# Optimization experiments

Hardware: AMD Instinct MI355X
Metric: run time of the kernel (lower is better)

## Reference

```python
import jax, jax.numpy as jnp
import numpy as np
import math

D_EMBED, D_K, N_HEADS = 1024, 1024, 16
D_H = D_EMBED // N_HEADS          # 64
ROT_DIM = D_H // 2                # 32, RotaryEmbedding(dim=d_h//2)
B, LQ, LK = 2, 2048, 2048


def _rope_freqs(seq_len):
    # lucidrains rotary-embedding-torch: inv_freq over half of `dim`, interleave-repeated
    inv_freq = 1.0 / (10000.0 ** (jnp.arange(0, ROT_DIM, 2, dtype=jnp.float32) / ROT_DIM))
    t = jnp.arange(seq_len, dtype=jnp.float32)
    f = t[:, None] * inv_freq[None, :]          # [S, ROT_DIM/2]
    return jnp.repeat(f, 2, axis=-1)            # [S, ROT_DIM] interleaved


def _apply_rotary(x, freqs):
    # x: [B,H,S,D_H]; rotate first ROT_DIM features, pass the rest through
    x_rot, x_pass = x[..., :ROT_DIM], x[..., ROT_DIM:]
    cos, sin = jnp.cos(freqs), jnp.sin(freqs)   # [S, ROT_DIM]
    x1, x2 = x_rot[..., 0::2], x_rot[..., 1::2]
    rotated = jnp.stack((-x2, x1), axis=-1).reshape(x_rot.shape)
    return jnp.concatenate([x_rot * cos + rotated * sin, x_pass], axis=-1)


def setup_inputs() -> dict:
    key = jax.random.key(0)
    ks = jax.random.split(key, 12)
    s = 0.02
    return {
        "embed": jax.random.normal(ks[0], (B, LQ, D_EMBED), jnp.float32),
        "key": jax.random.normal(ks[1], (B, LK, D_K), jnp.float32),
        "attn_mask": jnp.ones((B, LQ, LK), dtype=bool),
        "WQ": jax.random.normal(ks[2], (D_EMBED, D_EMBED), jnp.float32) * s,
        "bQ": jnp.zeros((D_EMBED,), jnp.float32),
        "WK": jax.random.normal(ks[3], (D_K, D_EMBED), jnp.float32) * s,
        "bK": jnp.zeros((D_EMBED,), jnp.float32),
        "WV": jax.random.normal(ks[4], (D_K, D_EMBED), jnp.float32) * s,
        "bV": jnp.zeros((D_EMBED,), jnp.float32),
        "WO": jax.random.normal(ks[5], (D_EMBED, D_EMBED), jnp.float32) * s,
        "bO": jnp.zeros((D_EMBED,), jnp.float32),
    }


def reference(embed, key, attn_mask, WQ, bQ, WK, bK, WV, bV, WO, bO):
    bsz, len_q, _ = embed.shape
    len_k = key.shape[1]
    scale = 1.0 / math.sqrt(D_EMBED)  # note: module scales by 1/sqrt(d_embed)

    Q = embed @ WQ + bQ
    K = key @ WK + bK
    V = key @ WV + bV

    # [B, H, S, D_H]
    Qh = Q.reshape(bsz, len_q, N_HEADS, D_H).transpose(0, 2, 1, 3)
    Kh = K.reshape(bsz, len_k, N_HEADS, D_H).transpose(0, 2, 1, 3)
    Vh = V.reshape(bsz, len_k, N_HEADS, D_H).transpose(0, 2, 1, 3)

    Qh = _apply_rotary(Qh, _rope_freqs(len_q))
    Kh = _apply_rotary(Kh, _rope_freqs(len_k))

    attn = jnp.einsum('bhqd,bhkd->bhqk', Qh, Kh)
    attn = jnp.where(attn_mask[:, None, :, :], attn, -jnp.inf)
    attn = jax.nn.softmax(attn * scale, axis=-1)

    out = jnp.einsum('bhqk,bhkd->bhqd', attn, Vh)
    out = out.transpose(0, 2, 1, 3).reshape(bsz, len_q, D_EMBED)
    return out @ WO + bO
```

## Files before the change

kernel.cpp:

```cpp
#include <hip/hip_runtime.h>
#include <hip/hip_bf16.h>
#include <cstdint>
#include <cstddef>

typedef __bf16 bf16_t;
typedef bf16_t bf16x8 __attribute__((ext_vector_type(8)));
typedef bf16_t bf16x4 __attribute__((ext_vector_type(4)));
typedef bf16_t bf16x2 __attribute__((ext_vector_type(2)));
typedef float f32x4 __attribute__((ext_vector_type(4)));
typedef float f32x16 __attribute__((ext_vector_type(16)));
typedef unsigned int u32x4 __attribute__((ext_vector_type(4)));

namespace {
constexpr int Bv = 2, Lv = 2048, Ev = 1024, NHv = 16;
constexpr int Mv = Bv * Lv;
constexpr float SCALE_L2E = 0.03125f * 1.4426950408889634f;
}

__device__ __forceinline__ void gload_lds16(const void* g, void* l) {
  __builtin_amdgcn_global_load_lds(
      (const __attribute__((address_space(1))) unsigned int*)g,
      (__attribute__((address_space(3))) unsigned int*)l,
      16, 0, 0);
}

__global__ __launch_bounds__(256) void k_cvt2(const float* __restrict__ x0,
                                              const float* __restrict__ x1,
                                              bf16_t* __restrict__ y0,
                                              bf16_t* __restrict__ y1, int n4) {
  const float* x = blockIdx.z ? x1 : x0;
  bf16_t* y = blockIdx.z ? y1 : y0;
  int i = blockIdx.x * 256 + threadIdx.x;
  if (i < n4) {
    float4 v = reinterpret_cast<const float4*>(x)[i];
    bf16x4 o = {(bf16_t)v.x, (bf16_t)v.y, (bf16_t)v.z, (bf16_t)v.w};
    *reinterpret_cast<bf16x4*>(&y[(size_t)i * 4]) = o;
  }
}

__global__ __launch_bounds__(256) void k_twt(const float* w0, const float* w1,
                                             const float* w2, const float* w3,
                                             bf16_t* t0, bf16_t* t1,
                                             bf16_t* t2, bf16_t* t3) {
  const float* W;
  bf16_t* T;
  switch (blockIdx.z) {
    case 0: W = w0; T = t0; break;
    case 1: W = w1; T = t1; break;
    case 2: W = w2; T = t2; break;
    default: W = w3; T = t3; break;
  }
  __shared__ float tile[32][33];
  const int tx = threadIdx.x, ty = threadIdx.y;
  const int n0 = blockIdx.x * 32, k0 = blockIdx.y * 32;
#pragma unroll
  for (int i = 0; i < 4; i++) {
    int r = ty + i * 8;
    tile[r][tx] = W[(size_t)(k0 + r) * Ev + n0 + tx];
  }
  __syncthreads();
#pragma unroll
  for (int i = 0; i < 4; i++) {
    int r = ty + i * 8;
    T[(size_t)(n0 + r) * Ev + k0 + tx] = (bf16_t)tile[tx][r];
  }
}

__global__ __launch_bounds__(256) void k_trig(float2* __restrict__ tab) {
  int t = blockIdx.x * 256 + threadIdx.x;
  int i = t & 15, l = t >> 4;
  float inv = exp2f(-13.287712379549449f * (float)i * (1.0f / 16.0f));
  float s, c;
  sincosf((float)l * inv, &s, &c);
  tab[t] = make_float2(c, s);
}

__global__ __launch_bounds__(256) void k_gemm_qkv(
    const bf16_t* __restrict__ Ae, const bf16_t* __restrict__ Ak,
    const bf16_t* __restrict__ WtQ, const bf16_t* __restrict__ WtK,
    const bf16_t* __restrict__ WtV, const float* __restrict__ bQ,
    const float* __restrict__ bK, const float* __restrict__ bV,
    const float2* __restrict__ tab, bf16_t* __restrict__ Qbf,
    bf16_t* __restrict__ Kbf, bf16_t* __restrict__ Vtr) {
  constexpr int K = Ev;
  const int z = blockIdx.z;
  const bf16_t* A = (z == 0) ? Ae : Ak;
  const bf16_t* Bt = (z == 0) ? WtQ : (z == 1) ? WtK : WtV;
  const float* bias = (z == 0) ? bQ : (z == 1) ? bK : bV;

  __shared__ __align__(16) bf16_t As[128 * 32];
  __shared__ __align__(16) bf16_t Bs[128 * 32];
  const int tid = threadIdx.x;
  const int wid = tid >> 6, lane = tid & 63;
  const int bm = blockIdx.y * 128, bn = blockIdx.x * 128;
  const int wr = wid >> 1, wc = wid & 1;
  f32x4 acc[4][4] = {};
  const int srow = wid * 32 + (lane >> 2);
  const int scol = (lane & 3) * 8;
  const size_t ga0 = (size_t)(bm + srow) * K + scol;
  const size_t ga1 = (size_t)(bm + srow + 16) * K + scol;
  const size_t gb0 = (size_t)(bn + srow) * K + scol;
  const size_t gb1 = (size_t)(bn + srow + 16) * K + scol;
  bf16_t* asw = &As[wid * 1024];
  bf16_t* bsw = &Bs[wid * 1024];
  for (int k0 = 0; k0 < K; k0 += 32) {
    gload_lds16(A + ga0 + k0, asw);
    gload_lds16(A + ga1 + k0, asw + 512);
    gload_lds16(Bt + gb0 + k0, bsw);
    gload_lds16(Bt + gb1 + k0, bsw + 512);
    __syncthreads();
    bf16x8 af[4], bfr[4];
#pragma unroll
    for (int m = 0; m < 4; m++)
      af[m] = *(const bf16x8*)&As[(wr * 64 + m * 16 + (lane & 15)) * 32 + (lane >> 4) * 8];
#pragma unroll
    for (int n = 0; n < 4; n++)
      bfr[n] = *(const bf16x8*)&Bs[(wc * 64 + n * 16 + (lane & 15)) * 32 + (lane >> 4) * 8];
#pragma unroll
    for (int m = 0; m < 4; m++)
#pragma unroll
      for (int n = 0; n < 4; n++)
        acc[m][n] = __builtin_amdgcn_mfma_f32_16x16x32_bf16(af[m], bfr[n], acc[m][n], 0, 0, 0);
    __syncthreads();
  }

  const int l15 = lane & 15, g = lane >> 4;
  if (z == 2) {
#pragma unroll
    for (int n = 0; n < 4; n++) {
      const int col = bn + wc * 64 + n * 16 + l15;
      const int hh = (col >> 6) & 15;
      const int d = col & 63;
      const float bv = bias[col];
#pragma unroll
      for (int m = 0; m < 4; m++) {
        const int row0 = bm + wr * 64 + m * 16 + (g << 2);
        const int b = row0 >> 11, l0 = row0 & 2047;
        const int pq = (l0 >> 2) & 3;
        const int pq2 = ((pq & 1) << 1) | (pq >> 1);
        const int l0p = (l0 & ~12) | (pq2 << 2);
        bf16x4 ov;
#pragma unroll
        for (int r = 0; r < 4; r++) ov[r] = (bf16_t)(acc[m][n][r] + bv);
        *(bf16x4*)&Vtr[((size_t)((b * NHv + hh) * 64 + d)) * Lv + l0p] = ov;
      }
    }
    return;
  }

  bf16_t* Y = (z == 0) ? Qbf : Kbf;
  const float scale = (z == 0) ? SCALE_L2E : 1.0f;
  const float ssign = (l15 & 1) ? 1.0f : -1.0f;
#pragma unroll
  for (int n = 0; n < 4; n++) {
    const int col = bn + wc * 64 + n * 16 + l15;
    const int h = (col >> 6) & 15;
    const int d = col & 63;
    const float bv = bias[col];
    const bool dorope = (d < 32);
    const int ti = d >> 1;
#pragma unroll
    for (int m = 0; m < 4; m++) {
      const int row0 = bm + wr * 64 + m * 16 + (g << 2);
#pragma unroll
      for (int r = 0; r < 4; r++) {
        const int row = row0 + r;
        const int l = row & 2047, b = row >> 11;
        float v = acc[m][n][r] + bv;
        float p = __shfl_xor(v, 1);
        float o = v;
        if (dorope) {
          float2 cs = tab[(l << 4) + ti];
          o = v * cs.x + p * cs.y * ssign;
        }
        Y[(((size_t)(b * NHv + h)) * Lv + l) * 64 + d] = (bf16_t)(o * scale);
      }
    }
  }
}

__global__ __launch_bounds__(256) void k_gemm_bt(const bf16_t* __restrict__ A,
                                                 const bf16_t* __restrict__ Bt,
                                                 const float* __restrict__ bias,
                                                 float* __restrict__ C,
                                                 int N, int K) {
  __shared__ __align__(16) bf16_t As[128 * 32];
  __shared__ __align__(16) bf16_t Bs[128 * 32];
  const int tid = threadIdx.x;
  const int wid = tid >> 6, lane = tid & 63;
  const int bm = blockIdx.y * 128, bn = blockIdx.x * 128;
  const int wr = wid >> 1, wc = wid & 1;
  f32x4 acc[4][4] = {};
  const int srow = wid * 32 + (lane >> 2);
  const int scol = (lane & 3) * 8;
  const size_t ga0 = (size_t)(bm + srow) * K + scol;
  const size_t ga1 = (size_t)(bm + srow + 16) * K + scol;
  const size_t gb0 = (size_t)(bn + srow) * K + scol;
  const size_t gb1 = (size_t)(bn + srow + 16) * K + scol;
  bf16_t* asw = &As[wid * 1024];
  bf16_t* bsw = &Bs[wid * 1024];
  for (int k0 = 0; k0 < K; k0 += 32) {
    gload_lds16(A + ga0 + k0, asw);
    gload_lds16(A + ga1 + k0, asw + 512);
    gload_lds16(Bt + gb0 + k0, bsw);
    gload_lds16(Bt + gb1 + k0, bsw + 512);
    __syncthreads();
    bf16x8 af[4], bfr[4];
#pragma unroll
    for (int m = 0; m < 4; m++)
      af[m] = *(const bf16x8*)&As[(wr * 64 + m * 16 + (lane & 15)) * 32 + (lane >> 4) * 8];
#pragma unroll
    for (int n = 0; n < 4; n++)
      bfr[n] = *(const bf16x8*)&Bs[(wc * 64 + n * 16 + (lane & 15)) * 32 + (lane >> 4) * 8];
#pragma unroll
    for (int m = 0; m < 4; m++)
#pragma unroll
      for (int n = 0; n < 4; n++)
        acc[m][n] = __builtin_amdgcn_mfma_f32_16x16x32_bf16(af[m], bfr[n], acc[m][n], 0, 0, 0);
    __syncthreads();
  }
#pragma unroll
  for (int n = 0; n < 4; n++) {
    const int col = bn + wc * 64 + n * 16 + (lane & 15);
    const float bv = bias[col];
#pragma unroll
    for (int m = 0; m < 4; m++) {
      const int row0 = bm + wr * 64 + m * 16 + ((lane >> 4) << 2);
#pragma unroll
      for (int r = 0; r < 4; r++)
        C[(size_t)(row0 + r) * N + col] = acc[m][n][r] + bv;
    }
  }
}

__global__ void k_flag_init(int* f) { f[0] = 1; f[1] = 1; }

__global__ __launch_bounds__(256) void k_mask_and(const unsigned int* __restrict__ m,
                                                  int* __restrict__ f, int nwords) {
  int i = blockIdx.x * 256 + threadIdx.x;
  const int u8words = nwords >> 2;
  bool badA = false, badB = false;
  for (; i < nwords; i += gridDim.x * 256) {
    unsigned int v = m[i];
    badA |= (i < u8words) & (v != 0x01010101u);
    badB |= (v != 1u);
  }
  if (__any(badA) && (threadIdx.x & 63) == 0) f[0] = 0;
  if (__any(badB) && (threadIdx.x & 63) == 0) f[1] = 0;
}

__device__ __forceinline__ void flash_stage(const bf16_t* __restrict__ Kg,
                                            const bf16_t* __restrict__ Vg,
                                            bf16_t* ksb, bf16_t* vsb,
                                            int tid, int kt) {
#pragma unroll
  for (int i = 0; i < 2; i++) {
    int slot = i * 256 + tid;
    int r = slot >> 3, c = slot & 7;
    int sb = ((c * 16) ^ ((r & 7) << 4)) >> 1;
    bf16_t* dk = ksb + (size_t)(i * 256 + (tid & 192)) * 8;
    gload_lds16(Kg + (size_t)(kt * 64 + r) * 64 + sb, dk);
    bf16_t* dv = vsb + (size_t)(i * 256 + (tid & 192)) * 8;
    gload_lds16(Vg + (size_t)r * Lv + kt * 64 + sb, dv);
  }
}

__global__ __launch_bounds__(256) void k_flash32(const bf16_t* __restrict__ Qh,
                                                 const bf16_t* __restrict__ Kh,
                                                 const bf16_t* __restrict__ Vtr,
                                                 const int* __restrict__ mask,
                                                 const int* __restrict__ allflag,
                                                 bf16_t* __restrict__ Oh) {
  __shared__ __align__(16) bf16_t Ks[2][64 * 64];
  __shared__ __align__(16) bf16_t Vs[2][64 * 64];
  __shared__ float sw[4][32];
  const int tid = threadIdx.x, wid = tid >> 6, lane = tid & 63;
  const int l31 = lane & 31, hf = lane >> 5;
  const int bh = blockIdx.x, qt = blockIdx.y;
  const int b = bh >> 4, hd = bh & 15;
  const size_t base = (size_t)bh * Lv * 64;
  const bf16_t* Kg = Kh + base;
  const bf16_t* Vg = Vtr + base;
  const int allm = allflag[0] | allflag[1];
  const int q = qt * 128 + wid * 32 + l31;

  bf16x8 bq[4];
#pragma unroll
  for (int s = 0; s < 4; s++)
    bq[s] = *(const bf16x8*)&Qh[base + (size_t)q * 64 + s * 16 + hf * 8];

  const int xsw = (l31 & 7) << 4;
  int eo_[4];
#pragma unroll
  for (int s = 0; s < 4; s++) eo_[s] = (((s * 16 + hf * 8) * 2) ^ xsw) >> 1;

  float m_r = -INFINITY, l_p = 0.f;
  f32x16 o0 = {}, o1 = {};

  flash_stage(Kg, Vg, Ks[0], Vs[0], tid, 0);
  __syncthreads();
  int cur = 0;
  for (int kt = 0; kt < Lv / 64; ++kt) {
    if (kt + 1 < Lv / 64)
      flash_stage(Kg, Vg, Ks[cur ^ 1], Vs[cur ^ 1], tid, kt + 1);
    const bf16_t* KsC = Ks[cur];
    const bf16_t* VsC = Vs[cur];

    f32x16 st0 = {}, st1 = {};
    __builtin_amdgcn_s_setprio(1);
#pragma unroll
    for (int s = 0; s < 4; s++) {
      bf16x8 k0 = *(const bf16x8*)&KsC[l31 * 64 + eo_[s]];
      bf16x8 k1 = *(const bf16x8*)&KsC[(32 + l31) * 64 + eo_[s]];
      st0 = __builtin_amdgcn_mfma_f32_32x32x16_bf16(k0, bq[s], st0, 0, 0, 0);
      st1 = __builtin_amdgcn_mfma_f32_32x32x16_bf16(k1, bq[s], st1, 0, 0, 0);
    }
    __builtin_amdgcn_s_setprio(0);

    if (!allm) {
      const int* mrow = &mask[(size_t)b * Lv * Lv + (size_t)q * Lv + kt * 64];
#pragma unroll
      for (int r = 0; r < 16; r++) {
        const int kv = (r & 3) + 8 * (r >> 2) + 4 * hf;
        if (!mrow[kv]) st0[r] = -INFINITY;
        if (!mrow[32 + kv]) st1[r] = -INFINITY;
      }
    }

    float pm = st0[0];
#pragma unroll
    for (int r = 1; r < 16; r++) pm = fmaxf(pm, st0[r]);
#pragma unroll
    for (int r = 0; r < 16; r++) pm = fmaxf(pm, st1[r]);
    if (__any(pm > m_r + 8.0f)) {
      float pmf = fmaxf(pm, __shfl_xor(pm, 32));
      float mn = fmaxf(m_r, pmf);
      float alpha = exp2f(m_r - mn);
      m_r = mn;
      l_p *= alpha;
      if (!hf) sw[wid][l31] = alpha;
      asm volatile("s_waitcnt lgkmcnt(0)" ::: "memory");
      __builtin_amdgcn_sched_barrier(0);
#pragma unroll
      for (int r = 0; r < 16; r++) {
        float a = sw[wid][(r & 3) + 8 * (r >> 2) + 4 * hf];
        o0[r] *= a;
        o1[r] *= a;
      }
    }
    float ps = 0.f;
#pragma unroll
    for (int r = 0; r < 16; r++) {
      float p = exp2f(st0[r] - m_r);
      st0[r] = p;
      ps += p;
    }
#pragma unroll
    for (int r = 0; r < 16; r++) {
      float p = exp2f(st1[r] - m_r);
      st1[r] = p;
      ps += p;
    }
    l_p += ps;

    unsigned int pk0[8], pk1[8];
#pragma unroll
    for (int i = 0; i < 8; i++) {
      float a0 = st0[2 * i], a1 = st0[2 * i + 1];
      float b0 = st1[2 * i], b1 = st1[2 * i + 1];
      asm("v_cvt_pk_bf16_f32 %0, %1, %2" : "=v"(pk0[i]) : "v"(a0), "v"(a1));
      asm("v_cvt_pk_bf16_f32 %0, %1, %2" : "=v"(pk1[i]) : "v"(b0), "v"(b1));
    }

    __builtin_amdgcn_s_setprio(1);
#pragma unroll
    for (int s = 0; s < 4; s++) {
      u32x4 u;
      if (s == 0) {
        u[0] = pk0[0]; u[1] = pk0[1]; u[2] = pk0[2]; u[3] = pk0[3];
      } else if (s == 1) {
        u[0] = pk0[4]; u[1] = pk0[5]; u[2] = pk0[6]; u[3] = pk0[7];
      } else if (s == 2) {
        u[0] = pk1[0]; u[1] = pk1[1]; u[2] = pk1[2]; u[3] = pk1[3];
      } else {
        u[0] = pk1[4]; u[1] = pk1[5]; u[2] = pk1[6]; u[3] = pk1[7];
      }
      bf16x8 pa = __builtin_bit_cast(bf16x8, u);
      bf16x8 v0 = *(const bf16x8*)&VsC[l31 * 64 + eo_[s]];
      bf16x8 v1 = *(const bf16x8*)&VsC[(32 + l31) * 64 + eo_[s]];
      o0 = __builtin_amdgcn_mfma_f32_32x32x16_bf16(pa, v0, o0, 0, 0, 0);
      o1 = __builtin_amdgcn_mfma_f32_32x32x16_bf16(pa, v1, o1, 0, 0, 0);
    }
    __builtin_amdgcn_s_setprio(0);

    __syncthreads();
    cur ^= 1;
  }

  float lt = l_p + __shfl_xor(l_p, 32);
  if (!hf) sw[wid][l31] = 1.0f / lt;
  asm volatile("s_waitcnt lgkmcnt(0)" ::: "memory");
  __builtin_amdgcn_sched_barrier(0);
#pragma unroll
  for (int r = 0; r < 16; r++) {
    const int rq = (r & 3) + 8 * (r >> 2) + 4 * hf;
    float inv = sw[wid][rq];
    const int qg = qt * 128 + wid * 32 + rq;
    const size_t off = ((size_t)(b * Lv + qg)) * Ev + hd * 64;
    Oh[off + l31] = (bf16_t)(o0[r] * inv);
    Oh[off + 32 + l31] = (bf16_t)(o1[r] * inv);
  }
}

extern "C" void kernel_launch(void* const* d_in, const int* in_sizes, int n_in,
                              void* d_out, int out_size, void* d_ws, size_t ws_size,
                              hipStream_t stream) {
  const float* embed = (const float*)d_in[0];
  const float* key = (const float*)d_in[1];
  const int* mask = (const int*)d_in[2];
  const float* WQ = (const float*)d_in[3];
  const float* bQ = (const float*)d_in[4];
  const float* WK = (const float*)d_in[5];
  const float* bK = (const float*)d_in[6];
  const float* WV = (const float*)d_in[7];
  const float* bV = (const float*)d_in[8];
  const float* WO = (const float*)d_in[9];
  const float* bO = (const float*)d_in[10];
  float* out = (float*)d_out;
  char* ws = (char*)d_ws;
  const size_t MB = 1024 * 1024;

  bf16_t* Wt = (bf16_t*)(ws);
  bf16_t* Ae = (bf16_t*)(ws + 8 * MB);
  bf16_t* Ak = (bf16_t*)(ws + 16 * MB);
  bf16_t* Qbf = (bf16_t*)(ws + 40 * MB);
  bf16_t* Kbf = (bf16_t*)(ws + 48 * MB);
  bf16_t* Vtr = (bf16_t*)(ws + 56 * MB);
  bf16_t* AO = (bf16_t*)(ws + 8 * MB);
  int* flag = (int*)(ws + 64 * MB);
  float2* tab = (float2*)(ws + 65 * MB);

  {
    dim3 cg(4096, 1, 2);
    k_cvt2<<<cg, 256, 0, stream>>>(embed, key, Ae, Ak, Mv * Ev / 4);
  }
  {
    dim3 tb(32, 8), tg(32, 32, 4);
    k_twt<<<tg, tb, 0, stream>>>(WQ, WK, WV, WO, Wt, Wt + 1024 * 1024,
                                 Wt + 2 * 1024 * 1024, Wt + 3 * 1024 * 1024);
  }
  k_trig<<<128, 256, 0, stream>>>(tab);
  k_flag_init<<<1, 1, 0, stream>>>(flag);
  k_mask_and<<<2048, 256, 0, stream>>>((const unsigned int*)mask, flag,
                                       Bv * Lv * Lv);

  {
    dim3 gg(8, 32, 3);
    k_gemm_qkv<<<gg, 256, 0, stream>>>(Ae, Ak, Wt, Wt + 1024 * 1024,
                                       Wt + 2 * 1024 * 1024, bQ, bK, bV, tab,
                                       Qbf, Kbf, Vtr);
  }
  {
    dim3 fg(32, 16);
    k_flash32<<<fg, 256, 0, stream>>>(Qbf, Kbf, Vtr, mask, flag, AO);
  }
  {
    dim3 gg(8, 32);
    k_gemm_bt<<<gg, 256, 0, stream>>>(AO, Wt + 3 * 1024 * 1024, bO, out, Ev, Ev);
  }
}
```

Baseline: 171.9 us.

## Fuse preprocessing kernels into one launch and shrink output GEMM N-tile

Merges input conversion, weight transpose, RoPE table generation and the mask-check scan into a single k_prep kernel that dispatches on block index. The flag init kernel is replaced by a memset, and the flags are inverted to mark bad mask formats, so the fast path is chosen the same way as before. The output projection GEMM tile goes from 128x128 to 128x64, which doubles the block count to fill the CUs better, at the cost of less reuse of A. The row-max reduction in the flash kernel is also reshaped into paired fmax steps to shorten the dependency chain.

```diff
diff --git a/kernel.cpp b/kernel.cpp
--- a/kernel.cpp
+++ b/kernel.cpp
@@ -24,55 +24,75 @@
       16, 0, 0);
 }
 
-__global__ __launch_bounds__(256) void k_cvt2(const float* __restrict__ x0,
-                                              const float* __restrict__ x1,
-                                              bf16_t* __restrict__ y0,
-                                              bf16_t* __restrict__ y1, int n4) {
-  const float* x = blockIdx.z ? x1 : x0;
-  bf16_t* y = blockIdx.z ? y1 : y0;
-  int i = blockIdx.x * 256 + threadIdx.x;
-  if (i < n4) {
+__global__ __launch_bounds__(256) void k_prep(
+    const float* __restrict__ embed, const float* __restrict__ key,
+    bf16_t* __restrict__ Ae, bf16_t* __restrict__ Ak,
+    float2* __restrict__ tab, int* __restrict__ bad,
+    const unsigned int* __restrict__ m,
+    const float* w0, const float* w1, const float* w2, const float* w3,
+    bf16_t* t0, bf16_t* t1, bf16_t* t2, bf16_t* t3) {
+  const int tid = threadIdx.x;
+  int bx = blockIdx.x;
+  if (bx < 8192) {
+    const float* x = (bx < 4096) ? embed : key;
+    bf16_t* y = (bx < 4096) ? Ae : Ak;
+    int i = (bx & 4095) * 256 + tid;
     float4 v = reinterpret_cast<const float4*>(x)[i];
     bf16x4 o = {(bf16_t)v.x, (bf16_t)v.y, (bf16_t)v.z, (bf16_t)v.w};
     *reinterpret_cast<bf16x4*>(&y[(size_t)i * 4]) = o;
-  }
-}
-
-__global__ __launch_bounds__(256) void k_twt(const float* w0, const float* w1,
-                                             const float* w2, const float* w3,
-                                             bf16_t* t0, bf16_t* t1,
-                                             bf16_t* t2, bf16_t* t3) {
-  const float* W;
-  bf16_t* T;
-  switch (blockIdx.z) {
-    case 0: W = w0; T = t0; break;
-    case 1: W = w1; T = t1; break;
-    case 2: W = w2; T = t2; break;
-    default: W = w3; T = t3; break;
-  }
-  __shared__ float tile[32][33];
-  const int tx = threadIdx.x, ty = threadIdx.y;
-  const int n0 = blockIdx.x * 32, k0 = blockIdx.y * 32;
-#pragma unroll
-  for (int i = 0; i < 4; i++) {
-    int r = ty + i * 8;
-    tile[r][tx] = W[(size_t)(k0 + r) * Ev + n0 + tx];
-  }
-  __syncthreads();
-#pragma unroll
-  for (int i = 0; i < 4; i++) {
-    int r = ty + i * 8;
-    T[(size_t)(n0 + r) * Ev + k0 + tx] = (bf16_t)tile[tx][r];
-  }
-}
-
-__global__ __launch_bounds__(256) void k_trig(float2* __restrict__ tab) {
-  int t = blockIdx.x * 256 + threadIdx.x;
-  int i = t & 15, l = t >> 4;
-  float inv = exp2f(-13.287712379549449f * (float)i * (1.0f / 16.0f));
-  float s, c;
-  sincosf((float)l * inv, &s, &c);
-  tab[t] = make_float2(c, s);
+    return;
+  }
+  bx -= 8192;
+  if (bx < 128) {
+    int t = bx * 256 + tid;
+    int i = t & 15, l = t >> 4;
+    float inv = exp2f(-13.287712379549449f * (float)i * (1.0f / 16.0f));
+    float s, c;
+    sincosf((float)l * inv, &s, &c);
+    tab[t] = make_float2(c, s);
+    return;
+  }
+  bx -= 128;
+  if (bx < 2048) {
+    const int nwords = Bv * Lv * Lv;
+    const int u8words = nwords >> 2;
+    int i = bx * 256 + tid;
+    bool badA = false, badB = false;
+    for (; i < nwords; i += 2048 * 256) {
+      unsigned int v = m[i];
+      badA |= (i < u8words) & (v != 0x01010101u);
+      badB |= (v != 1u);
+    }
+    if (__any(badA) && (tid & 63) == 0) bad[0] = 1;
+    if (__any(badB) && (tid & 63) == 0) bad[1] = 1;
+    return;
+  }
+  bx -= 2048;
+  {
+    const int z = bx >> 10, rem = bx & 1023;
+    const float* W;
+    bf16_t* T;
+    switch (z) {
+      case 0: W = w0; T = t0; break;
+      case 1: W = w1; T = t1; break;
+      case 2: W = w2; T = t2; break;
+      default: W = w3; T = t3; break;
+    }
+    __shared__ float tile[32][33];
+    const int tx = tid & 31, ty = tid >> 5;
+    const int n0 = (rem & 31) * 32, k0 = (rem >> 5) * 32;
+#pragma unroll
+    for (int i = 0; i < 4; i++) {
+      int r = ty + i * 8;
+      tile[r][tx] = W[(size_t)(k0 + r) * Ev + n0 + tx];
+    }
+    __syncthreads();
+#pragma unroll
+    for (int i = 0; i < 4; i++) {
+      int r = ty + i * 8;
+      T[(size_t)(n0 + r) * Ev + k0 + tx] = (bf16_t)tile[tx][r];
+    }
+  }
 }
 
 __global__ __launch_bounds__(256) void k_gemm_qkv(
@@ -185,43 +205,42 @@
                                                  float* __restrict__ C,
                                                  int N, int K) {
   __shared__ __align__(16) bf16_t As[128 * 32];
-  __shared__ __align__(16) bf16_t Bs[128 * 32];
+  __shared__ __align__(16) bf16_t Bs[64 * 32];
   const int tid = threadIdx.x;
   const int wid = tid >> 6, lane = tid & 63;
-  const int bm = blockIdx.y * 128, bn = blockIdx.x * 128;
+  const int bm = blockIdx.y * 128, bn = blockIdx.x * 64;
   const int wr = wid >> 1, wc = wid & 1;
-  f32x4 acc[4][4] = {};
-  const int srow = wid * 32 + (lane >> 2);
+  f32x4 acc[4][2] = {};
+  const int srowA = wid * 32 + (lane >> 2);
+  const int srowB = wid * 16 + (lane >> 2);
   const int scol = (lane & 3) * 8;
-  const size_t ga0 = (size_t)(bm + srow) * K + scol;
-  const size_t ga1 = (size_t)(bm + srow + 16) * K + scol;
-  const size_t gb0 = (size_t)(bn + srow) * K + scol;
-  const size_t gb1 = (size_t)(bn + srow + 16) * K + scol;
+  const size_t ga0 = (size_t)(bm + srowA) * K + scol;
+  const size_t ga1 = (size_t)(bm + srowA + 16) * K + scol;
+  const size_t gb0 = (size_t)(bn + srowB) * K + scol;
   bf16_t* asw = &As[wid * 1024];
-  bf16_t* bsw = &Bs[wid * 1024];
+  bf16_t* bsw = &Bs[wid * 512];
   for (int k0 = 0; k0 < K; k0 += 32) {
     gload_lds16(A + ga0 + k0, asw);
     gload_lds16(A + ga1 + k0, asw + 512);
     gload_lds16(Bt + gb0 + k0, bsw);
-    gload_lds16(Bt + gb1 + k0, bsw + 512);
-    __syncthreads();
-    bf16x8 af[4], bfr[4];
+    __syncthreads();
+    bf16x8 af[4], bfr[2];
 #pragma unroll
     for (int m = 0; m < 4; m++)
       af[m] = *(const bf16x8*)&As[(wr * 64 + m * 16 + (lane & 15)) * 32 + (lane >> 4) * 8];
 #pragma unroll
-    for (int n = 0; n < 4; n++)
-      bfr[n] = *(const bf16x8*)&Bs[(wc * 64 + n * 16 + (lane & 15)) * 32 + (lane >> 4) * 8];
+    for (int n = 0; n < 2; n++)
+      bfr[n] = *(const bf16x8*)&Bs[(wc * 32 + n * 16 + (lane & 15)) * 32 + (lane >> 4) * 8];
 #pragma unroll
     for (int m = 0; m < 4; m++)
 #pragma unroll
-      for (int n = 0; n < 4; n++)
+      for (int n = 0; n < 2; n++)
         acc[m][n] = __builtin_amdgcn_mfma_f32_16x16x32_bf16(af[m], bfr[n], acc[m][n], 0, 0, 0);
     __syncthreads();
   }
 #pragma unroll
-  for (int n = 0; n < 4; n++) {
-    const int col = bn + wc * 64 + n * 16 + (lane & 15);
+  for (int n = 0; n < 2; n++) {
+    const int col = bn + wc * 32 + n * 16 + (lane & 15);
     const float bv = bias[col];
 #pragma unroll
     for (int m = 0; m < 4; m++) {
@@ -231,22 +250,6 @@
         C[(size_t)(row0 + r) * N + col] = acc[m][n][r] + bv;
     }
   }
-}
-
-__global__ void k_flag_init(int* f) { f[0] = 1; f[1] = 1; }
-
-__global__ __launch_bounds__(256) void k_mask_and(const unsigned int* __restrict__ m,
-                                                  int* __restrict__ f, int nwords) {
-  int i = blockIdx.x * 256 + threadIdx.x;
-  const int u8words = nwords >> 2;
-  bool badA = false, badB = false;
-  for (; i < nwords; i += gridDim.x * 256) {
-    unsigned int v = m[i];
-    badA |= (i < u8words) & (v != 0x01010101u);
-    badB |= (v != 1u);
-  }
-  if (__any(badA) && (threadIdx.x & 63) == 0) f[0] = 0;
-  if (__any(badB) && (threadIdx.x & 63) == 0) f[1] = 0;
 }
 
 __device__ __forceinline__ void flash_stage(const bf16_t* __restrict__ Kg,
@@ -269,7 +272,7 @@
                                                  const bf16_t* __restrict__ Kh,
                                                  const bf16_t* __restrict__ Vtr,
                                                  const int* __restrict__ mask,
-                                                 const int* __restrict__ allflag,
+                                                 const int* __restrict__ bad,
                                                  bf16_t* __restrict__ Oh) {
   __shared__ __align__(16) bf16_t Ks[2][64 * 64];
   __shared__ __align__(16) bf16_t Vs[2][64 * 64];
@@ -281,7 +284,7 @@
   const size_t base = (size_t)bh * Lv * 64;
   const bf16_t* Kg = Kh + base;
   const bf16_t* Vg = Vtr + base;
-  const int allm = allflag[0] | allflag[1];
+  const int allm = !(bad[0] & bad[1]);
   const int q = qt * 128 + wid * 32 + l31;
 
   bf16x8 bq[4];
@@ -327,11 +330,11 @@
       }
     }
 
-    float pm = st0[0];
-#pragma unroll
-    for (int r = 1; r < 16; r++) pm = fmaxf(pm, st0[r]);
-#pragma unroll
-    for (int r = 0; r < 16; r++) pm = fmaxf(pm, st1[r]);
+    float pm = fmaxf(st0[0], st0[1]);
+#pragma unroll
+    for (int r = 2; r < 16; r += 2) pm = fmaxf(fmaxf(st0[r], st0[r + 1]), pm);
+#pragma unroll
+    for (int r = 0; r < 16; r += 2) pm = fmaxf(fmaxf(st1[r], st1[r + 1]), pm);
     if (__any(pm > m_r + 8.0f)) {
       float pmf = fmaxf(pm, __shfl_xor(pm, 32));
       float mn = fmaxf(m_r, pmf);
@@ -437,22 +440,14 @@
   bf16_t* Kbf = (bf16_t*)(ws + 48 * MB);
   bf16_t* Vtr = (bf16_t*)(ws + 56 * MB);
   bf16_t* AO = (bf16_t*)(ws + 8 * MB);
-  int* flag = (int*)(ws + 64 * MB);
+  int* bad = (int*)(ws + 64 * MB);
   float2* tab = (float2*)(ws + 65 * MB);
 
-  {
-    dim3 cg(4096, 1, 2);
-    k_cvt2<<<cg, 256, 0, stream>>>(embed, key, Ae, Ak, Mv * Ev / 4);
-  }
-  {
-    dim3 tb(32, 8), tg(32, 32, 4);
-    k_twt<<<tg, tb, 0, stream>>>(WQ, WK, WV, WO, Wt, Wt + 1024 * 1024,
-                                 Wt + 2 * 1024 * 1024, Wt + 3 * 1024 * 1024);
-  }
-  k_trig<<<128, 256, 0, stream>>>(tab);
-  k_flag_init<<<1, 1, 0, stream>>>(flag);
-  k_mask_and<<<2048, 256, 0, stream>>>((const unsigned int*)mask, flag,
-                                       Bv * Lv * Lv);
+  hipMemsetAsync(bad, 0, 2 * sizeof(int), stream);
+  k_prep<<<14464, 256, 0, stream>>>(embed, key, Ae, Ak, tab, bad,
+                                    (const unsigned int*)mask, WQ, WK, WV, WO,
+                                    Wt, Wt + 1024 * 1024, Wt + 2 * 1024 * 1024,
+                                    Wt + 3 * 1024 * 1024);
 
   {
     dim3 gg(8, 32, 3);
@@ -462,10 +457,10 @@
   }
   {
     dim3 fg(32, 16);
-    k_flash32<<<fg, 256, 0, stream>>>(Qbf, Kbf, Vtr, mask, flag, AO);
+    k_flash32<<<fg, 256, 0, stream>>>(Qbf, Kbf, Vtr, mask, bad, AO);
   }
   {
-    dim3 gg(8, 32);
+    dim3 gg(16, 32);
     k_gemm_bt<<<gg, 256, 0, stream>>>(AO, Wt + 3 * 1024 * 1024, bO, out, Ev, Ev);
   }
 }
```

Result: faster. 161.9 us (median of 3 runs) (-5.8%).
